# Kernel optimization log

Hardware: AMD Instinct MI355X
Metric: run time of the kernel (lower is better)

Reference implementation:

```python
import jax, jax.numpy as jnp
import numpy as np
from jax import lax

N = 10000
E = 320000
FLAT = 32 * 10 * 32  # conv channels * pooled 20x64 -> 10x32


def setup_inputs() -> dict:
    key = jax.random.key(0)
    ks = jax.random.split(key, 16)
    s = 0.05
    return {
        "features": jax.random.normal(ks[0], (N, 20, 64), jnp.float32),
        "src": jax.random.randint(ks[1], (E,), 0, N, jnp.int32),
        "dst": jax.random.randint(ks[2], (E,), 0, N, jnp.int32),
        # CNN params
        "conv_w": jax.random.normal(ks[3], (32, 1, 3, 3), jnp.float32) * s,
        "conv_b": jnp.zeros((32,), jnp.float32),
        "w1": jax.random.normal(ks[4], (FLAT, 32), jnp.float32) * s,
        "b1": jnp.zeros((32,), jnp.float32),
        "w2": jax.random.normal(ks[5], (32, 32), jnp.float32) * s,
        "b2": jnp.zeros((32,), jnp.float32),
        # SAGEConv1 (32 -> 64)
        "s1_self": jax.random.normal(ks[6], (32, 64), jnp.float32) * s,
        "s1_neigh": jax.random.normal(ks[7], (32, 64), jnp.float32) * s,
        "s1_b": jnp.zeros((64,), jnp.float32),
        # SAGEConv2 (64 -> 10)
        "s2_self": jax.random.normal(ks[8], (64, 10), jnp.float32) * s,
        "s2_neigh": jax.random.normal(ks[9], (64, 10), jnp.float32) * s,
        "s2_b": jnp.zeros((10,), jnp.float32),
    }


def _cnn(x, conv_w, conv_b, w1, b1, w2, b2):
    # x: [N, 1, 20, 64]
    x = lax.conv_general_dilated(x, conv_w, (1, 1), "SAME",
                                 dimension_numbers=("NCHW", "OIHW", "NCHW"))
    x = jax.nn.relu(x + conv_b[None, :, None, None])
    x = lax.reduce_window(x, -jnp.inf, lax.max, (1, 1, 2, 2), (1, 1, 2, 2), "VALID")
    x = x.reshape(x.shape[0], -1)  # [N, FLAT], NCHW flatten matches torch
    x = jax.nn.relu(x @ w1 + b1)
    x = jax.nn.relu(x @ w2 + b2)
    return x


def _sage_mean(x, src, dst, w_self, w_neigh, b):
    # DGL SAGEConv 'mean': mean over in-neighbors (messages src->dst)
    agg = jax.ops.segment_sum(x[src], dst, num_segments=N)
    deg = jax.ops.segment_sum(jnp.ones((src.shape[0],), x.dtype), dst, num_segments=N)
    agg = agg / jnp.maximum(deg, 1.0)[:, None]
    return x @ w_self + agg @ w_neigh + b


def reference(features, src, dst, conv_w, conv_b, w1, b1, w2, b2,
              s1_self, s1_neigh, s1_b, s2_self, s2_neigh, s2_b):
    h = _cnn(features[:, None, :, :], conv_w, conv_b, w1, b1, w2, b2)  # [N, 32]
    h = jax.nn.relu(_sage_mean(h, src, dst, s1_self, s1_neigh, s1_b))  # [N, 64]
    out = _sage_mean(h, src, dst, s2_self, s2_neigh, s2_b)             # [N, 10]
    return out
```

## Files before the change

kernel.cpp:

```cpp
#include <hip/hip_runtime.h>


typedef __attribute__((ext_vector_type(8)))  short bf16x8;
typedef __attribute__((ext_vector_type(4)))  float f32x4;
typedef __attribute__((ext_vector_type(16))) float f32x16;

__device__ __forceinline__ unsigned short f2bf(float v) {
    union { float f; unsigned int u; } x; x.f = v;
    unsigned int r = x.u + 0x7FFFu + ((x.u >> 16) & 1u);
    return (unsigned short)(r >> 16);
}
__device__ __forceinline__ float bf2f(unsigned short b) {
    union { float f; unsigned int u; } x; x.u = ((unsigned int)b) << 16;
    return x.f;
}
__device__ __forceinline__ unsigned cvtpk(float a, float b) {
    unsigned r;
    asm("v_cvt_pk_bf16_f32 %0, %1, %2" : "=v"(r) : "v"(a), "v"(b));
    return r;
}
__device__ __forceinline__ float lo2f(unsigned p) { union { unsigned u; float f; } x; x.u = p << 16; return x.f; }
__device__ __forceinline__ float hi2f(unsigned p) { union { unsigned u; float f; } x; x.u = p & 0xffff0000u; return x.f; }
__device__ __forceinline__ void split_pair(float a, float b, unsigned& hp, unsigned& lp) {
    hp = cvtpk(a, b);
    lp = cvtpk(a - lo2f(hp), b - hi2f(hp));
}

__global__ __launch_bounds__(256) void zero_ws(float* __restrict__ ws, int count) {
    int i = blockIdx.x * 256 + threadIdx.x;
    if (i < count) ws[i] = 0.0f;
}

__global__ __launch_bounds__(256) void w1_prep_v3(
    const float* __restrict__ w1, unsigned char* __restrict__ w1f)
{
    int gu = blockIdx.x * 256 + threadIdx.x;
    const int quarter = gu >> 11;
    const int u = gu & 2047;
    const int ph = quarter >> 2, qq = quarter & 3;
    const int ks   = u >> 8;
    const int jh   = (u >> 7) & 1;
    const int part = (u >> 6) & 1;
    const int lane = u & 63;
    const int j    = jh * 16 + (lane & 15);
    const int c    = ks * 4 + (lane >> 4);
    const int k0   = c * 320 + ph * 32 + qq * 8;
    unsigned short v[8];
#pragma unroll
    for (int i = 0; i < 8; ++i) {
        float x = w1[(size_t)(k0 + i) * 32 + j];
        unsigned short h = f2bf(x);
        v[i] = part ? f2bf(x - bf2f(h)) : h;
    }
    *(uint4*)(w1f + (size_t)quarter * 32768 + (size_t)u * 16) = *(const uint4*)v;
}

__global__ __launch_bounds__(256, 4) void cnn_fused_v14(
    const float* __restrict__ feat,
    const float* __restrict__ conv_w, const float* __restrict__ conv_b,
    const unsigned char* __restrict__ w1f,
    float* __restrict__ h_fc1)
{
    __shared__ __align__(16) unsigned char convA[18432];
    __shared__ __align__(16) unsigned char fc1A[16384];

    const int t = threadIdx.x;
    const int wv = t >> 6;
    const int lane = t & 63;
    const int base = blockIdx.x * 16;
    const int qq = blockIdx.y;

    const int nn  = lane >> 4;
    const int pwl = lane & 7;
    const int aa  = (lane >> 3) & 1;
    const float* featn = feat + (size_t)(base + wv * 4 + nn) * 1280;

    const int pw = qq * 8 + pwl;
    const int c0 = 2 * pw - 1;
    const bool cv0 = (c0 >= 0);
    const bool cv3 = (c0 + 3 < 64);

    const int cch = lane & 31;
    const int ckg = lane >> 5;
    const int rowr = lane & 31;
    unsigned rsw = (unsigned)(rowr << 4); rsw ^= ((rsw >> 7) & 3u) << 4;

    bf16x8 cbh, cbl;
    {
        union { unsigned short u[8]; bf16x8 v; } H, L;
#pragma unroll
        for (int i = 0; i < 8; ++i) {
            int k = ckg * 8 + i;
            float x = (k < 9) ? conv_w[cch * 9 + k] : (k == 9 ? conv_b[cch] : 0.0f);
            unsigned short h = f2bf(x);
            H.u[i] = h; L.u[i] = f2bf(x - bf2f(h));
        }
        cbh = H.v; cbl = L.v;
    }

    const int nfr = lane & 15;

    f32x4 acc0 = {0.f, 0.f, 0.f, 0.f};
    f32x4 acc1 = {0.f, 0.f, 0.f, 0.f};
    const f32x16 czero = {};

    float f0[4], f1[4], f2[4];
    auto load_row = [&](int r, float* o) {
        bool rv = (r >= 0) && (r < 20);
        const float* rp = featn + (rv ? r : 0) * 64;
        float2 m = *(const float2*)(rp + c0 + 1);
        float v0 = rp[cv0 ? c0 : 0];
        float v3 = rp[cv3 ? (c0 + 3) : 0];
        o[0] = (rv && cv0) ? v0 : 0.f;
        o[1] = rv ? m.x : 0.f;
        o[2] = rv ? m.y : 0.f;
        o[3] = (rv && cv3) ? v3 : 0.f;
    };

    load_row(aa - 1, f0);
    load_row(aa,     f1);
    load_row(aa + 1, f2);

#pragma unroll 1
    for (int ph = 0; ph < 10; ++ph) {
        const int quarter = ph * 4 + qq;
        unsigned char* fbuf = fc1A;

        const unsigned char* wq = w1f + (size_t)quarter * 32768;
        bf16x8 bF[2][2][2];
#pragma unroll
        for (int si = 0; si < 2; ++si) {
            const int ks = wv + si * 4;
#pragma unroll
            for (int jh = 0; jh < 2; ++jh)
#pragma unroll
                for (int part = 0; part < 2; ++part)
                    bF[si][jh][part] = *(const bf16x8*)(
                        wq + (size_t)((((ks * 2 + jh) * 2 + part)) << 10) + lane * 16);
        }

        {
            unsigned P[3][2], Q[3][2];
            split_pair(f0[0], f0[1], P[0][0], Q[0][0]);
            split_pair(f0[2], f0[3], P[0][1], Q[0][1]);
            split_pair(f1[0], f1[1], P[1][0], Q[1][0]);
            split_pair(f1[2], f1[3], P[1][1], Q[1][1]);
            split_pair(f2[0], f2[1], P[2][0], Q[2][0]);
            split_pair(f2[2], f2[3], P[2][1], Q[2][1]);

            const int r0 = pwl * 4 + aa * 2, r1 = r0 + 1;
            unsigned b0 = (unsigned)(r0 << 4); b0 ^= ((b0 >> 7) & 3u) << 4;
            unsigned b1 = (unsigned)(r1 << 4); b1 ^= ((b1 >> 7) & 3u) << 4;
            unsigned char* abw = convA + ((wv * 4 + nn) << 10);
            uint4 H0 = make_uint4(P[0][0],
                                  __builtin_amdgcn_perm(P[1][0], P[0][1], 0x05040100u),
                                  __builtin_amdgcn_perm(P[1][1], P[1][0], 0x05040302u),
                                  P[2][0]);
            uint4 H1 = make_uint4(__builtin_amdgcn_perm(P[0][1], P[0][0], 0x05040302u),
                                  __builtin_amdgcn_perm(P[1][0], P[0][1], 0x07060302u),
                                  P[1][1],
                                  __builtin_amdgcn_perm(P[2][1], P[2][0], 0x05040302u));
            uint4 L0 = make_uint4(Q[0][0],
                                  __builtin_amdgcn_perm(Q[1][0], Q[0][1], 0x05040100u),
                                  __builtin_amdgcn_perm(Q[1][1], Q[1][0], 0x05040302u),
                                  Q[2][0]);
            uint4 L1 = make_uint4(__builtin_amdgcn_perm(Q[0][1], Q[0][0], 0x05040302u),
                                  __builtin_amdgcn_perm(Q[1][0], Q[0][1], 0x07060302u),
                                  Q[1][1],
                                  __builtin_amdgcn_perm(Q[2][1], Q[2][0], 0x05040302u));
            *(uint4*)(abw + b0)       = H0;
            *(uint4*)(abw + b1)       = H1;
            *(uint4*)(abw + 512 + b0) = L0;
            *(uint4*)(abw + 512 + b1) = L1;
            unsigned wr0 = __builtin_amdgcn_perm(Q[2][1], P[2][1], 0x05040100u);
            unsigned wr1 = __builtin_amdgcn_perm(Q[2][1], P[2][1], 0x07060302u);
            *(uint2*)(convA + 16384 + (((wv * 4 + nn) * 32 + r0) << 2)) = make_uint2(wr0, wr1);
        }

        if (ph < 9) {
#pragma unroll
            for (int j = 0; j < 4; ++j) f0[j] = f2[j];
            load_row(2 * ph + 2 + aa, f1);
            load_row(2 * ph + 3 + aa, f2);
        }

#pragma unroll
        for (int nn2 = 0; nn2 < 4; ++nn2) {
            bf16x8 a_h, a_l;
            if (ckg == 0) {
                const unsigned char* ab = convA + ((wv * 4 + nn2) << 10);
                a_h = *(const bf16x8*)(ab + rsw);
                a_l = *(const bf16x8*)(ab + 512 + rsw);
            } else {
                unsigned cw = *(const unsigned*)(convA + 16384 + (((wv * 4 + nn2) * 32 + rowr) << 2));
                a_h = (bf16x8){(short)(cw & 0xffffu), (short)0x3F80, 0, 0, 0, 0, 0, 0};
                a_l = (bf16x8){(short)(cw >> 16),     0,             0, 0, 0, 0, 0, 0};
            }
            f32x16 ca;
            ca = __builtin_amdgcn_mfma_f32_32x32x16_bf16(a_l, cbh, czero, 0, 0, 0);
            ca = __builtin_amdgcn_mfma_f32_32x32x16_bf16(a_h, cbl, ca, 0, 0, 0);
            ca = __builtin_amdgcn_mfma_f32_32x32x16_bf16(a_h, cbh, ca, 0, 0, 0);

            float pv0 = fmaxf(fmaxf(fmaxf(ca[0],  ca[1]),  fmaxf(ca[2],  ca[3])),  0.f);
            float pv1 = fmaxf(fmaxf(fmaxf(ca[4],  ca[5]),  fmaxf(ca[6],  ca[7])),  0.f);
            float pv2 = fmaxf(fmaxf(fmaxf(ca[8],  ca[9]),  fmaxf(ca[10], ca[11])), 0.f);
            float pv3 = fmaxf(fmaxf(fmaxf(ca[12], ca[13]), fmaxf(ca[14], ca[15])), 0.f);

            unsigned ha, la, hb, lb;
            split_pair(pv0, pv1, ha, la);
            split_pair(pv2, pv3, hb, lb);
            unsigned pha = (unsigned)__shfl_xor((int)ha, 32);
            unsigned phb = (unsigned)__shfl_xor((int)hb, 32);
            unsigned pla = (unsigned)__shfl_xor((int)la, 32);
            unsigned plb = (unsigned)__shfl_xor((int)lb, 32);
            bool hih = (lane < 32);
            unsigned q0v = hih ? pha : la;
            unsigned q1v = hih ? ha  : pla;
            unsigned q2v = hih ? phb : lb;
            unsigned q3v = hih ? hb  : plb;
            unsigned w0  = __builtin_amdgcn_perm(q0v, q1v, 0x05040100u);
            unsigned w1v = __builtin_amdgcn_perm(q0v, q1v, 0x07060302u);
            unsigned w2v = __builtin_amdgcn_perm(q2v, q3v, 0x05040100u);
            unsigned w3v = __builtin_amdgcn_perm(q2v, q3v, 0x07060302u);
            const int nloc = wv * 4 + nn2;
            const int pS = hih ? 0 : 1;
            const int ksW = cch >> 2, kgW = cch & 3;
            unsigned byteW = (unsigned)((((pS * 8 + ksW) * 64) + kgW * 16 + nloc) << 4);
            byteW ^= ((byteW >> 8) & 7u) << 4;
            *(uint4*)(fbuf + byteW) = make_uint4(w0, w1v, w2v, w3v);
        }

        __syncthreads();

#pragma unroll
        for (int si = 0; si < 2; ++si) {
            const int ks = wv + si * 4;
            unsigned bH = (unsigned)(((0 * 8 + ks) << 10) + lane * 16); bH ^= ((bH >> 8) & 7u) << 4;
            unsigned bL = (unsigned)(((1 * 8 + ks) << 10) + lane * 16); bL ^= ((bL >> 8) & 7u) << 4;
            bf16x8 fa_h = *(const bf16x8*)(fbuf + bH);
            bf16x8 fa_l = *(const bf16x8*)(fbuf + bL);
            acc0 = __builtin_amdgcn_mfma_f32_16x16x32_bf16(fa_l, bF[si][0][0], acc0, 0, 0, 0);
            acc0 = __builtin_amdgcn_mfma_f32_16x16x32_bf16(fa_h, bF[si][0][1], acc0, 0, 0, 0);
            acc0 = __builtin_amdgcn_mfma_f32_16x16x32_bf16(fa_h, bF[si][0][0], acc0, 0, 0, 0);
            acc1 = __builtin_amdgcn_mfma_f32_16x16x32_bf16(fa_l, bF[si][1][0], acc1, 0, 0, 0);
            acc1 = __builtin_amdgcn_mfma_f32_16x16x32_bf16(fa_h, bF[si][1][1], acc1, 0, 0, 0);
            acc1 = __builtin_amdgcn_mfma_f32_16x16x32_bf16(fa_h, bF[si][1][0], acc1, 0, 0, 0);
        }

        __syncthreads();
    }

    float* red = (float*)convA;
#pragma unroll
    for (int r = 0; r < 4; ++r) {
        int node = (lane >> 4) * 4 + r;
        red[wv * 512 + node * 32 + nfr]      = acc0[r];
        red[wv * 512 + node * 32 + 16 + nfr] = acc1[r];
    }
    __syncthreads();
    {
        const int en = t >> 4, jp = t & 15;
        const int j0 = 2 * jp;
        float s0 = 0.f, s1 = 0.f;
#pragma unroll
        for (int wi = 0; wi < 4; ++wi) {
            s0 += red[wi * 512 + en * 32 + j0];
            s1 += red[wi * 512 + en * 32 + j0 + 1];
        }
        atomicAdd(&h_fc1[(size_t)(base + en) * 32 + j0],     s0);
        atomicAdd(&h_fc1[(size_t)(base + en) * 32 + j0 + 1], s1);
    }
}

__global__ __launch_bounds__(256) void fc1_finish(
    const float* __restrict__ h_fc1, const float* __restrict__ b1,
    const float* __restrict__ w2, const float* __restrict__ b2,
    float* __restrict__ h_out, int N)
{
    __shared__ float hr[8][32];
    const int t = threadIdx.x;
    const int nb = t >> 5, j = t & 31;
    const int n = blockIdx.x * 8 + nb;
    if (n < N) hr[nb][j] = fmaxf(h_fc1[(size_t)n * 32 + j] + b1[j], 0.f);
    __syncthreads();
    if (n >= N) return;
    float o = b2[j];
#pragma unroll
    for (int k = 0; k < 32; ++k) o = fmaf(hr[nb][k], w2[k * 32 + j], o);
    h_out[(size_t)n * 32 + j] = fmaxf(o, 0.f);
}

__global__ __launch_bounds__(256) void count_deg(
    const int* __restrict__ dst, int* __restrict__ cnt, int E)
{
    int e = blockIdx.x * 256 + threadIdx.x;
    if (e < E) atomicAdd(&cnt[dst[e]], 1);
}

__global__ __launch_bounds__(256) void scan_local(
    const int* __restrict__ cnt, int* __restrict__ excl, int* __restrict__ bsum, int N)
{
    __shared__ int s[256];
    int t = threadIdx.x, b = blockIdx.x, i = b * 256 + t;
    int v = (i < N) ? cnt[i] : 0;
    s[t] = v;
    __syncthreads();
#pragma unroll
    for (int off = 1; off < 256; off <<= 1) {
        int x = (t >= off) ? s[t - off] : 0;
        __syncthreads();
        s[t] += x;
        __syncthreads();
    }
    int incl = s[t];
    if (i < N) excl[i] = incl - v;
    if (t == 255) bsum[b] = incl;
}

__global__ __launch_bounds__(64) void scan_bsum(
    const int* __restrict__ bsum, int* __restrict__ bsumx, int* __restrict__ row_ptr,
    int nb, int N)
{
    int t = threadIdx.x;
    int v = (t < nb) ? bsum[t] : 0;
    int incl = v;
#pragma unroll
    for (int off = 1; off < 64; off <<= 1) {
        int x = __shfl_up(incl, off);
        if (t >= off) incl += x;
    }
    if (t < nb) bsumx[t] = incl - v;
    if (t == 63) row_ptr[N] = incl;
}

__global__ __launch_bounds__(256) void scan_add(
    const int* __restrict__ excl, const int* __restrict__ bsumx,
    int* __restrict__ row_ptr, int* __restrict__ cursor, int N)
{
    int i = blockIdx.x * 256 + threadIdx.x;
    if (i < N) {
        int rp = excl[i] + bsumx[i >> 8];
        row_ptr[i] = rp;
        cursor[i]  = rp;
    }
}

__global__ __launch_bounds__(256) void fill_csr(
    const int* __restrict__ src, const int* __restrict__ dst,
    int* __restrict__ cursor, int* __restrict__ csr, int E)
{
    int e = blockIdx.x * 256 + threadIdx.x;
    if (e >= E) return;
    int idx = atomicAdd(&cursor[dst[e]], 1);
    csr[idx] = src[e];
}

__global__ __launch_bounds__(256) void sage1_fused(
    const float* __restrict__ h, const int* __restrict__ rp, const int* __restrict__ csr,
    const float* __restrict__ s1_self, const float* __restrict__ s1_neigh,
    const float* __restrict__ s1_b, const float* __restrict__ s2_neigh,
    float* __restrict__ h1, float* __restrict__ z16, int N)
{
    __shared__ float aggs[4][32];
    __shared__ float hl[4][64];
    const int t = threadIdx.x;
    const int nb = t >> 6, k = t & 63;
    const int n = blockIdx.x * 4 + nb;
    const int j = k & 31, half = k >> 5;

    int p0 = 0, p1 = 0;
    if (n < N) { p0 = rp[n]; p1 = rp[n + 1]; }
    float a = 0.f;
    for (int p = p0 + half; p < p1; p += 2)
        a += h[(size_t)csr[p] * 32 + j];
    a += __shfl_down(a, 32);
    if (half == 0) aggs[nb][j] = a;
    __syncthreads();

    float o = 0.f;
    if (n < N) {
        const int nu = __builtin_amdgcn_readfirstlane(n);
        float inv = 1.0f / fmaxf((float)(p1 - p0), 1.0f);
        o = s1_b[k];
#pragma unroll
        for (int jj = 0; jj < 32; ++jj) {
            o = fmaf(h[(size_t)nu * 32 + jj], s1_self[jj * 64 + k], o);
            o = fmaf(aggs[nb][jj] * inv, s1_neigh[jj * 64 + k], o);
        }
        o = fmaxf(o, 0.f);
        h1[(size_t)n * 64 + k] = o;
    }
    hl[nb][k] = o;
    __syncthreads();

    if (n < N && k < 16) {
        float z = 0.f;
        if (k < 10) {
#pragma unroll
            for (int jj = 0; jj < 64; ++jj) z = fmaf(hl[nb][jj], s2_neigh[jj * 10 + k], z);
        }
        z16[(size_t)n * 16 + k] = z;
    }
}

__global__ __launch_bounds__(256) void sage2_final_g(
    const float* __restrict__ h1, const float* __restrict__ z16,
    const int* __restrict__ rp, const int* __restrict__ csr,
    const float* __restrict__ s2_self, const float* __restrict__ s2_b,
    float* __restrict__ out, int N)
{
    int tid = blockIdx.x * 256 + threadIdx.x;
    int nn = tid >> 4, k = tid & 15;
    if (nn >= N || k >= 10) return;
    int p0 = rp[nn], p1 = rp[nn + 1];
    float a0 = 0.f, a1 = 0.f;
    int p = p0;
    for (; p + 2 <= p1; p += 2) {
        int s0 = csr[p], s1 = csr[p + 1];
        a0 += z16[(size_t)s0 * 16 + k];
        a1 += z16[(size_t)s1 * 16 + k];
    }
    if (p < p1) a0 += z16[(size_t)csr[p] * 16 + k];
    float inv = 1.0f / fmaxf((float)(p1 - p0), 1.0f);
    float o = s2_b[k] + (a0 + a1) * inv;
#pragma unroll
    for (int j = 0; j < 64; ++j) o = fmaf(h1[nn * 64 + j], s2_self[j * 10 + k], o);
    out[nn * 10 + k] = o;
}

extern "C" void kernel_launch(void* const* d_in, const int* in_sizes, int n_in,
                              void* d_out, int out_size, void* d_ws, size_t ws_size,
                              hipStream_t stream)
{
    const float* feat     = (const float*)d_in[0];
    const int*   src      = (const int*)d_in[1];
    const int*   dst      = (const int*)d_in[2];
    const float* conv_w   = (const float*)d_in[3];
    const float* conv_b   = (const float*)d_in[4];
    const float* w1       = (const float*)d_in[5];
    const float* b1       = (const float*)d_in[6];
    const float* w2       = (const float*)d_in[7];
    const float* b2       = (const float*)d_in[8];
    const float* s1_self  = (const float*)d_in[9];
    const float* s1_neigh = (const float*)d_in[10];
    const float* s1_b     = (const float*)d_in[11];
    const float* s2_self  = (const float*)d_in[12];
    const float* s2_neigh = (const float*)d_in[13];
    const float* s2_b     = (const float*)d_in[14];
    float* out = (float*)d_out;

    const int N = in_sizes[0] / 1280;
    const int E = in_sizes[1];
    const int NB_SCAN = (N + 255) / 256;

    char* wsb = (char*)d_ws;
    int*   row_cnt = (int*)wsb;                      wsb += (size_t)N * 4;
    float* h_fc1   = (float*)wsb;                    wsb += (size_t)N * 32 * 4;
    int*   excl    = (int*)wsb;                      wsb += (size_t)N * 4;
    int*   bsum    = (int*)wsb;                      wsb += 64 * 4;
    int*   bsumx   = (int*)wsb;                      wsb += 64 * 4;
    int*   row_ptr = (int*)wsb;                      wsb += (size_t)(N + 4) * 4;
    int*   cursor  = (int*)wsb;                      wsb += (size_t)N * 4;
    int*   csr     = (int*)wsb;                      wsb += (size_t)E * 4;
    float* h_cnn   = (float*)wsb;                    wsb += (size_t)N * 32 * 4;
    float* h1      = (float*)wsb;                    wsb += (size_t)N * 64 * 4;
    float* z16     = (float*)wsb;                    wsb += (size_t)N * 16 * 4;
    unsigned char* w1f = (unsigned char*)wsb;

    zero_ws<<<(33 * N + 255) / 256, 256, 0, stream>>>((float*)row_cnt, 33 * N);

    count_deg<<<(E + 255) / 256, 256, 0, stream>>>(dst, row_cnt, E);
    scan_local<<<NB_SCAN, 256, 0, stream>>>(row_cnt, excl, bsum, N);
    scan_bsum<<<1, 64, 0, stream>>>(bsum, bsumx, row_ptr, NB_SCAN, N);
    scan_add<<<NB_SCAN, 256, 0, stream>>>(excl, bsumx, row_ptr, cursor, N);
    fill_csr<<<(E + 255) / 256, 256, 0, stream>>>(src, dst, cursor, csr, E);

    w1_prep_v3<<<320, 256, 0, stream>>>(w1, w1f);
    dim3 cg(N / 16, 4);
    cnn_fused_v14<<<cg, 256, 0, stream>>>(feat, conv_w, conv_b, w1f, h_fc1);
    fc1_finish<<<(N + 7) / 8, 256, 0, stream>>>(h_fc1, b1, w2, b2, h_cnn, N);

    sage1_fused<<<(N + 3) / 4, 256, 0, stream>>>(
        h_cnn, row_ptr, csr, s1_self, s1_neigh, s1_b, s2_neigh, h1, z16, N);

    sage2_final_g<<<(int)(((size_t)N * 16 + 255) / 256), 256, 0, stream>>>(
        h1, z16, row_ptr, csr, s2_self, s2_b, out, N);
}
```

Before: 202.6 us.

## Split CNN phase loop across more blocks and precompute SAGE2 self term

Measured after the change: 216.6 us. 6.9% more time.

```diff
diff --git a/kernel.cpp b/kernel.cpp
--- a/kernel.cpp
+++ b/kernel.cpp
@@ -55,7 +55,7 @@
     *(uint4*)(w1f + (size_t)quarter * 32768 + (size_t)u * 16) = *(const uint4*)v;
 }
 
-__global__ __launch_bounds__(256, 4) void cnn_fused_v14(
+__global__ __launch_bounds__(256, 4) void cnn_fused_v15(
     const float* __restrict__ feat,
     const float* __restrict__ conv_w, const float* __restrict__ conv_b,
     const unsigned char* __restrict__ w1f,
@@ -68,7 +68,8 @@
     const int wv = t >> 6;
     const int lane = t & 63;
     const int base = blockIdx.x * 16;
-    const int qq = blockIdx.y;
+    const int qq = blockIdx.y & 3;
+    const int phlo = (blockIdx.y >> 2) * 5;
 
     const int nn  = lane >> 4;
     const int pwl = lane & 7;
@@ -117,12 +118,12 @@
         o[3] = (rv && cv3) ? v3 : 0.f;
     };
 
-    load_row(aa - 1, f0);
-    load_row(aa,     f1);
-    load_row(aa + 1, f2);
+    load_row(2 * phlo - 1 + aa, f0);
+    load_row(2 * phlo + aa,     f1);
+    load_row(2 * phlo + 1 + aa, f2);
 
 #pragma unroll 1
-    for (int ph = 0; ph < 10; ++ph) {
+    for (int ph = phlo; ph < phlo + 5; ++ph) {
         const int quarter = ph * 4 + qq;
         unsigned char* fbuf = fc1A;
 
@@ -177,7 +178,7 @@
             *(uint2*)(convA + 16384 + (((wv * 4 + nn) * 32 + r0) << 2)) = make_uint2(wr0, wr1);
         }
 
-        if (ph < 9) {
+        if (ph < phlo + 4) {
 #pragma unroll
             for (int j = 0; j < 4; ++j) f0[j] = f2[j];
             load_row(2 * ph + 2 + aa, f1);
@@ -359,7 +360,8 @@
     const float* __restrict__ h, const int* __restrict__ rp, const int* __restrict__ csr,
     const float* __restrict__ s1_self, const float* __restrict__ s1_neigh,
     const float* __restrict__ s1_b, const float* __restrict__ s2_neigh,
-    float* __restrict__ h1, float* __restrict__ z16, int N)
+    const float* __restrict__ s2_self, const float* __restrict__ s2_b,
+    float* __restrict__ z16, float* __restrict__ self16, int N)
 {
     __shared__ float aggs[4][32];
     __shared__ float hl[4][64];
@@ -388,25 +390,29 @@
             o = fmaf(aggs[nb][jj] * inv, s1_neigh[jj * 64 + k], o);
         }
         o = fmaxf(o, 0.f);
-        h1[(size_t)n * 64 + k] = o;
     }
     hl[nb][k] = o;
     __syncthreads();
 
-    if (n < N && k < 16) {
-        float z = 0.f;
+    if (n < N) {
         if (k < 10) {
+            float z = 0.f;
 #pragma unroll
             for (int jj = 0; jj < 64; ++jj) z = fmaf(hl[nb][jj], s2_neigh[jj * 10 + k], z);
-        }
-        z16[(size_t)n * 16 + k] = z;
+            z16[(size_t)n * 16 + k] = z;
+        } else if (k >= 16 && k < 26) {
+            const int kk = k - 16;
+            float s = s2_b[kk];
+#pragma unroll
+            for (int jj = 0; jj < 64; ++jj) s = fmaf(hl[nb][jj], s2_self[jj * 10 + kk], s);
+            self16[(size_t)n * 16 + kk] = s;
+        }
     }
 }
 
 __global__ __launch_bounds__(256) void sage2_final_g(
-    const float* __restrict__ h1, const float* __restrict__ z16,
+    const float* __restrict__ z16, const float* __restrict__ self16,
     const int* __restrict__ rp, const int* __restrict__ csr,
-    const float* __restrict__ s2_self, const float* __restrict__ s2_b,
     float* __restrict__ out, int N)
 {
     int tid = blockIdx.x * 256 + threadIdx.x;
@@ -422,10 +428,7 @@
     }
     if (p < p1) a0 += z16[(size_t)csr[p] * 16 + k];
     float inv = 1.0f / fmaxf((float)(p1 - p0), 1.0f);
-    float o = s2_b[k] + (a0 + a1) * inv;
-#pragma unroll
-    for (int j = 0; j < 64; ++j) o = fmaf(h1[nn * 64 + j], s2_self[j * 10 + k], o);
-    out[nn * 10 + k] = o;
+    out[nn * 10 + k] = self16[(size_t)nn * 16 + k] + (a0 + a1) * inv;
 }
 
 extern "C" void kernel_launch(void* const* d_in, const int* in_sizes, int n_in,
@@ -463,8 +466,8 @@
     int*   cursor  = (int*)wsb;                      wsb += (size_t)N * 4;
     int*   csr     = (int*)wsb;                      wsb += (size_t)E * 4;
     float* h_cnn   = (float*)wsb;                    wsb += (size_t)N * 32 * 4;
-    float* h1      = (float*)wsb;                    wsb += (size_t)N * 64 * 4;
     float* z16     = (float*)wsb;                    wsb += (size_t)N * 16 * 4;
+    float* self16  = (float*)wsb;                    wsb += (size_t)N * 16 * 4;
     unsigned char* w1f = (unsigned char*)wsb;
 
     zero_ws<<<(33 * N + 255) / 256, 256, 0, stream>>>((float*)row_cnt, 33 * N);
@@ -476,13 +479,14 @@
     fill_csr<<<(E + 255) / 256, 256, 0, stream>>>(src, dst, cursor, csr, E);
 
     w1_prep_v3<<<320, 256, 0, stream>>>(w1, w1f);
-    dim3 cg(N / 16, 4);
-    cnn_fused_v14<<<cg, 256, 0, stream>>>(feat, conv_w, conv_b, w1f, h_fc1);
+    dim3 cg(N / 16, 8);
+    cnn_fused_v15<<<cg, 256, 0, stream>>>(feat, conv_w, conv_b, w1f, h_fc1);
     fc1_finish<<<(N + 7) / 8, 256, 0, stream>>>(h_fc1, b1, w2, b2, h_cnn, N);
 
     sage1_fused<<<(N + 3) / 4, 256, 0, stream>>>(
-        h_cnn, row_ptr, csr, s1_self, s1_neigh, s1_b, s2_neigh, h1, z16, N);
+        h_cnn, row_ptr, csr, s1_self, s1_neigh, s1_b, s2_neigh, s2_self, s2_b,
+        z16, self16, N);
 
     sage2_final_g<<<(int)(((size_t)N * 16 + 255) / 256), 256, 0, stream>>>(
-        h1, z16, row_ptr, csr, s2_self, s2_b, out, N);
-}
+        z16, self16, row_ptr, csr, out, N);
+}
```
